# Optimization experiments

Hardware: AMD Instinct MI355X
Metric: run time of the kernel (lower is better)

Reference implementation:

```python
import jax, jax.numpy as jnp
import numpy as np

IDIM = 192
NB_SAMPLES = 128
NB_RAYS = 16384


def setup_inputs() -> dict:
    key = jax.random.key(0)
    k1, k2, k3, k4 = jax.random.split(key, 4)
    # origins strictly inside the AABB [0, idim-1]^3 so every ray intersects
    x = jax.random.uniform(k1, (NB_RAYS, 3), dtype=jnp.float32) * (IDIM - 2.0) + 0.5
    d = jax.random.normal(k2, (NB_RAYS, 3), dtype=jnp.float32)
    # keep components away from 0 so 1/d is finite, then normalize
    d = jnp.where(jnp.abs(d) < 1e-3, 1e-3, d)
    d = d / jnp.linalg.norm(d, axis=1, keepdims=True)
    grid = jax.random.uniform(k3, (IDIM, IDIM, IDIM, 9), dtype=jnp.float32)
    opacity = jax.random.uniform(k4, (IDIM, IDIM, IDIM), dtype=jnp.float32)
    return {"x": x, "d": d, "grid": grid, "opacity": opacity}


def _intersect_ray_aabb(x, inv_d, idim):
    inf = jnp.float32(idim) ** 3
    box_min = jnp.zeros((1, 3), jnp.float32)
    box_max = jnp.full((1, 3), jnp.float32(idim - 1))
    t0 = (box_min - x) * inv_d
    t1 = (box_max - x) * inv_d
    tsmaller = jnp.minimum(t0, t1)
    tbigger = jnp.maximum(t0, t1)
    tmin = jnp.maximum(-inf, jnp.max(tsmaller, axis=1))
    tmax = jnp.minimum(inf, jnp.min(tbigger, axis=1))
    return tmin, tmax


def _forward(x, d, grid, opacity):
    idim = grid.shape[0]
    R = x.shape[0]
    inv_d = 1.0 / d
    tmin, tmax = _intersect_ray_aabb(x, inv_d, idim)
    # Uniform(tmin, tmax) samples, sorted per ray (torch .sample() is no-grad)
    u = jax.random.uniform(jax.random.key(1), (R, NB_SAMPLES), dtype=jnp.float32)
    samples = jnp.sort(tmin[:, None] + u * (tmax - tmin)[:, None], axis=1)
    samples = jax.lax.stop_gradient(samples)

    # sample points along rays: [R, S, 3]
    pts = x[:, None, :] + samples[..., None] * d[:, None, :]
    i0 = jnp.clip(jnp.floor(pts).astype(jnp.int32), 0, idim - 2)  # base corner
    frac = pts - i0.astype(pts.dtype)  # trilinear weights (delta_voxel = 1)
    fx, fy, fz = frac[..., 0], frac[..., 1], frac[..., 2]
    ix, iy, iz = i0[..., 0], i0[..., 1], i0[..., 2]

    harm = jnp.zeros(pts.shape[:2] + (9,), pts.dtype)  # [R, S, 9]
    opac = jnp.zeros(pts.shape[:2], pts.dtype)         # [R, S]
    for ox in (0, 1):
        wx = fx if ox else (1.0 - fx)
        for oy in (0, 1):
            wy = fy if oy else (1.0 - fy)
            for oz in (0, 1):
                wz = fz if oz else (1.0 - fz)
                w = wx * wy * wz
                gi, gj, gk = ix + ox, iy + oy, iz + oz
                harm = harm + w[..., None] * grid[gi, gj, gk]
                opac = opac + w * opacity[gi, gj, gk]

    # volumetric compositing over the first S-1 samples (vectorized form of
    # the original sequential transmittance loop)
    deltas = samples[:, 1:] - samples[:, :-1]            # [R, S-1]
    cur = deltas * opac[:, :-1]                          # per-step opacity
    cum_excl = jnp.concatenate(
        [jnp.zeros((R, 1), cur.dtype), jnp.cumsum(cur, axis=1)[:, :-1]], axis=1)
    trans = jnp.exp(-cum_excl)
    color_s = jax.nn.sigmoid(jnp.sum(harm[:, :-1, :], axis=-1))
    rays_color = jnp.sum(trans * (1.0 - jnp.exp(-cur)) * color_s, axis=1)
    return rays_color


def reference(x, d, grid, opacity):
    return _forward(x, d, grid, opacity)
```

## Files before the change

### kernel.cpp

```cpp
#include <hip/hip_runtime.h>
#include <hip/hip_fp16.h>
#include <cstdint>
#include <cstddef>

#define IDIM 192
#define NSAMP 128
#define NRAYS 16384
#define NVOX (IDIM * IDIM * IDIM)


__device__ __forceinline__ uint32_t rotl32(uint32_t x, int r) {
    return (x << r) | (x >> (32 - r));
}

__device__ __forceinline__ uint32_t threefry_bits(uint32_t i) {
    const uint32_t ks0 = 0u;
    const uint32_t ks1 = 1u;
    const uint32_t ks2 = 0x1BD11BDAu ^ ks0 ^ ks1;
    uint32_t x0 = 0u + ks0;
    uint32_t x1 = i + ks1;
#define TF_ROUND(r) { x0 += x1; x1 = rotl32(x1, (r)); x1 ^= x0; }
    TF_ROUND(13) TF_ROUND(15) TF_ROUND(26) TF_ROUND(6)
    x0 += ks1; x1 += ks2 + 1u;
    TF_ROUND(17) TF_ROUND(29) TF_ROUND(16) TF_ROUND(24)
    x0 += ks2; x1 += ks0 + 2u;
    TF_ROUND(13) TF_ROUND(15) TF_ROUND(26) TF_ROUND(6)
    x0 += ks0; x1 += ks1 + 3u;
    TF_ROUND(17) TF_ROUND(29) TF_ROUND(16) TF_ROUND(24)
    x0 += ks1; x1 += ks2 + 4u;
    TF_ROUND(13) TF_ROUND(15) TF_ROUND(26) TF_ROUND(6)
    x0 += ks2; x1 += ks0 + 5u;
#undef TF_ROUND
    return x0 ^ x1;
}

__global__ __launch_bounds__(256)
void fuse_kernel(const float* __restrict__ grid, const float* __restrict__ opacity,
                 __half2* __restrict__ tab) {
    __shared__ float sh[256 * 9];
    const int t = threadIdx.x;
    const int base = blockIdx.x * 256;
    const float* gp = grid + (size_t)base * 9;
    #pragma unroll
    for (int i = 0; i < 9; ++i) {
        sh[i * 256 + t] = gp[i * 256 + t];
    }
    __syncthreads();
    float s = 0.f;
    #pragma unroll
    for (int c = 0; c < 9; ++c) s += sh[t * 9 + c];
    const int v = base + t;
    const int xq = v / (IDIM * IDIM);
    const int rem = v - xq * (IDIM * IDIM);
    const int yq = rem / IDIM;
    const int zq = rem - yq * IDIM;
    const int idx = (xq >> 1) * 73728 + ((xq & 1) << 3)
                  + (yq >> 1) * 768   + ((yq & 1) << 2)
                  + (zq >> 2) * 16    + (zq & 3);
    tab[idx] = __floats2half2_rn(s, opacity[v]);
}

__global__ __launch_bounds__(128, 8)
void rf_kernel(const float* __restrict__ x, const float* __restrict__ d,
               const __half2* __restrict__ tab, float* __restrict__ out) {
    const int wave = threadIdx.x >> 6;
    const int lane = threadIdx.x & 63;
    const int r = blockIdx.x * 2 + wave;

    const float ox = x[r * 3 + 0], oy = x[r * 3 + 1], oz = x[r * 3 + 2];
    const float dx = d[r * 3 + 0], dy = d[r * 3 + 1], dz = d[r * 3 + 2];
    const float inv_dx = 1.f / dx, inv_dy = 1.f / dy, inv_dz = 1.f / dz;
    const float INF = 7077888.f;
    const float BMAX = (float)(IDIM - 1);

    float tmin = -INF, tmax = INF;
    {
        float t0 = (0.f - ox) * inv_dx, t1 = (BMAX - ox) * inv_dx;
        tmin = fmaxf(tmin, fminf(t0, t1)); tmax = fminf(tmax, fmaxf(t0, t1));
        t0 = (0.f - oy) * inv_dy; t1 = (BMAX - oy) * inv_dy;
        tmin = fmaxf(tmin, fminf(t0, t1)); tmax = fminf(tmax, fmaxf(t0, t1));
        t0 = (0.f - oz) * inv_dz; t1 = (BMAX - oz) * inv_dz;
        tmin = fmaxf(tmin, fminf(t0, t1)); tmax = fminf(tmax, fmaxf(t0, t1));
    }

    const uint32_t i0 = (uint32_t)(r * NSAMP + lane);
    const uint32_t b0 = threefry_bits(i0);
    const uint32_t b1 = threefry_bits(i0 + 64u);
    float u0 = __uint_as_float((b0 >> 9) | 0x3f800000u) - 1.0f;
    float u1 = __uint_as_float((b1 >> 9) | 0x3f800000u) - 1.0f;
    u0 = fmaxf(0.f, u0);
    u1 = fmaxf(0.f, u1);
    float v0 = tmin + u0 * (tmax - tmin);
    float v1 = tmin + u1 * (tmax - tmin);

#define BSTEP(J, K)                                                            \
    {                                                                          \
        const float p0 = __shfl_xor(v0, (J));                                  \
        const float p1 = __shfl_xor(v1, (J));                                  \
        const bool lower = (lane & (J)) == 0;                                  \
        const bool tm0 = (((lane) & (K)) == 0) == lower;                       \
        const bool tm1 = ((((lane) + 64) & (K)) == 0) == lower;                \
        v0 = tm0 ? fminf(v0, p0) : fmaxf(v0, p0);                              \
        v1 = tm1 ? fminf(v1, p1) : fmaxf(v1, p1);                              \
    }
    #pragma unroll
    for (int k = 2; k <= 64; k <<= 1) {
        #pragma unroll
        for (int j = k >> 1; j >= 1; j >>= 1) BSTEP(j, k)
    }
    {
        const float mn = fminf(v0, v1), mx = fmaxf(v0, v1);
        v0 = mn; v1 = mx;
    }
    #pragma unroll
    for (int j = 32; j >= 1; j >>= 1) BSTEP(j, 128)
#undef BSTEP

    auto sample_tab = [&](float tpar, float& hsv, float& opv) {
        const float px = ox + tpar * dx;
        const float py = oy + tpar * dy;
        const float pz = oz + tpar * dz;
        int ix = (int)floorf(px); ix = ix < 0 ? 0 : (ix > IDIM - 2 ? IDIM - 2 : ix);
        int iy = (int)floorf(py); iy = iy < 0 ? 0 : (iy > IDIM - 2 ? IDIM - 2 : iy);
        int iz = (int)floorf(pz); iz = iz < 0 ? 0 : (iz > IDIM - 2 ? IDIM - 2 : iz);
        const float fx = px - (float)ix;
        const float fy = py - (float)iy;
        const float fz = pz - (float)iz;
        const float wx0 = 1.f - fx, wx1 = fx;
        const float wy0 = 1.f - fy, wy1 = fy;
        const float wz0 = 1.f - fz, wz1 = fz;
        const float w000 = wx0 * wy0 * wz0, w001 = wx0 * wy0 * wz1;
        const float w010 = wx0 * wy1 * wz0, w011 = wx0 * wy1 * wz1;
        const float w100 = wx1 * wy0 * wz0, w101 = wx1 * wy0 * wz1;
        const float w110 = wx1 * wy1 * wz0, w111 = wx1 * wy1 * wz1;
        const int f0 = (ix >> 1) * 73728 + ((ix & 1) << 3);
        const int f1 = ((ix + 1) >> 1) * 73728 + (((ix + 1) & 1) << 3);
        const int g0 = (iy >> 1) * 768 + ((iy & 1) << 2);
        const int g1 = ((iy + 1) >> 1) * 768 + (((iy + 1) & 1) << 2);
        const int h0 = (iz >> 2) * 16 + (iz & 3);
        const int h1 = ((iz + 1) >> 2) * 16 + ((iz + 1) & 3);
        const float2 c000 = __half22float2(tab[f0 + g0 + h0]);
        const float2 c001 = __half22float2(tab[f0 + g0 + h1]);
        const float2 c010 = __half22float2(tab[f0 + g1 + h0]);
        const float2 c011 = __half22float2(tab[f0 + g1 + h1]);
        const float2 c100 = __half22float2(tab[f1 + g0 + h0]);
        const float2 c101 = __half22float2(tab[f1 + g0 + h1]);
        const float2 c110 = __half22float2(tab[f1 + g1 + h0]);
        const float2 c111 = __half22float2(tab[f1 + g1 + h1]);
        hsv = w000 * c000.x + w001 * c001.x + w010 * c010.x + w011 * c011.x +
              w100 * c100.x + w101 * c101.x + w110 * c110.x + w111 * c111.x;
        opv = w000 * c000.y + w001 * c001.y + w010 * c010.y + w011 * c011.y +
              w100 * c100.y + w101 * c101.y + w110 * c110.y + w111 * c111.y;
    };

    const float ts = v0;
    const float sd0 = __shfl_down(v0, 1);
    const float b64 = __shfl(v1, 0);
    const float tn = (lane < 63) ? sd0 : b64;

    float hsv, opv;
    sample_tab(ts, hsv, opv);
    const float cur = (tn - ts) * opv;

    float incl = cur;
    #pragma unroll
    for (int off = 1; off < 64; off <<= 1) {
        const float tmp = __shfl_up(incl, off);
        if (lane >= off) incl += tmp;
    }
    const float excl = incl - cur;
    const float color = 1.f / (1.f + __expf(-hsv));
    float contrib = __expf(-excl) * (1.f - __expf(-cur)) * color;

    float red = contrib;
    #pragma unroll
    for (int off = 32; off > 0; off >>= 1) red += __shfl_down(red, off);
    float total = red;

    const float cum64 = __shfl(incl, 63);

    if (cum64 < 10.f) {
        const bool act = lane < 63;
        const float ts2 = v1;
        const float tn2 = __shfl_down(v1, 1);
        float hsv2, opv2;
        sample_tab(ts2, hsv2, opv2);
        const float cur2 = act ? (tn2 - ts2) * opv2 : 0.f;

        float incl2 = cur2;
        #pragma unroll
        for (int off = 1; off < 64; off <<= 1) {
            const float tmp = __shfl_up(incl2, off);
            if (lane >= off) incl2 += tmp;
        }
        const float excl2 = cum64 + (incl2 - cur2);
        const float color2 = 1.f / (1.f + __expf(-hsv2));
        float c2 = act ? __expf(-excl2) * (1.f - __expf(-cur2)) * color2 : 0.f;
        #pragma unroll
        for (int off = 32; off > 0; off >>= 1) c2 += __shfl_down(c2, off);
        total += c2;
    }

    if (lane == 0) out[r] = total;
}

extern "C" void kernel_launch(void* const* d_in, const int* in_sizes, int n_in,
                              void* d_out, int out_size, void* d_ws, size_t ws_size,
                              hipStream_t stream) {
    const float* x       = (const float*)d_in[0];
    const float* d       = (const float*)d_in[1];
    const float* grid    = (const float*)d_in[2];
    const float* opacity = (const float*)d_in[3];
    float* out = (float*)d_out;

    fuse_kernel<<<NVOX / 256, 256, 0, stream>>>(grid, opacity, (__half2*)d_ws);
    rf_kernel<<<NRAYS / 2, 128, 0, stream>>>(x, d, (const __half2*)d_ws, out);
}
```

Baseline: 79.16 us.

## Split trilinear corners across lane pairs and process samples in four chunks

Each pair of lanes now handles one sample: each lane gathers the four corners on its x side and the pair combines partial sums with a lane shuffle. The ray is processed in four chunks of 32 samples with a running transmittance sum and an early exit once accumulated opacity passes a threshold. The intent is to halve the gather work per lane and add finer-grained early termination. In exchange there are more scan passes and shuffles, and half the lanes sit idle in the compositing step.

Measured after the change: 77.90 us. No clear change (-1.6%).

```diff
diff --git a/kernel.cpp b/kernel.cpp
--- a/kernel.cpp
+++ b/kernel.cpp
@@ -116,92 +116,74 @@
     for (int j = 32; j >= 1; j >>= 1) BSTEP(j, 128)
 #undef BSTEP
 
-    auto sample_tab = [&](float tpar, float& hsv, float& opv) {
-        const float px = ox + tpar * dx;
-        const float py = oy + tpar * dy;
-        const float pz = oz + tpar * dz;
+    const int odd = lane & 1;
+    const int hs  = lane >> 1;
+    float cumRay = 0.f, acc = 0.f;
+
+    for (int k = 0; k < 4; ++k) {
+        const int sk = k * 32 + hs;
+        const bool valid = (sk < NSAMP - 1);
+
+        float ts, tn;
+        if (k < 2) {
+            ts = __shfl(v0, sk);
+            const float tnv = __shfl(v0, (sk + 1 > 63) ? 63 : sk + 1);
+            const float s64 = __shfl(v1, 0);
+            tn = (sk == 63) ? s64 : tnv;
+        } else {
+            ts = __shfl(v1, sk - 64);
+            const int ti = sk - 63;
+            tn = __shfl(v1, (ti > 63) ? 63 : ti);
+        }
+
+        const float px = ox + ts * dx;
+        const float py = oy + ts * dy;
+        const float pz = oz + ts * dz;
         int ix = (int)floorf(px); ix = ix < 0 ? 0 : (ix > IDIM - 2 ? IDIM - 2 : ix);
         int iy = (int)floorf(py); iy = iy < 0 ? 0 : (iy > IDIM - 2 ? IDIM - 2 : iy);
         int iz = (int)floorf(pz); iz = iz < 0 ? 0 : (iz > IDIM - 2 ? IDIM - 2 : iz);
         const float fx = px - (float)ix;
         const float fy = py - (float)iy;
         const float fz = pz - (float)iz;
-        const float wx0 = 1.f - fx, wx1 = fx;
+        const float wxs = odd ? fx : (1.f - fx);
         const float wy0 = 1.f - fy, wy1 = fy;
         const float wz0 = 1.f - fz, wz1 = fz;
-        const float w000 = wx0 * wy0 * wz0, w001 = wx0 * wy0 * wz1;
-        const float w010 = wx0 * wy1 * wz0, w011 = wx0 * wy1 * wz1;
-        const float w100 = wx1 * wy0 * wz0, w101 = wx1 * wy0 * wz1;
-        const float w110 = wx1 * wy1 * wz0, w111 = wx1 * wy1 * wz1;
-        const int f0 = (ix >> 1) * 73728 + ((ix & 1) << 3);
-        const int f1 = ((ix + 1) >> 1) * 73728 + (((ix + 1) & 1) << 3);
+        const int xs = ix + odd;
+        const int fs = (xs >> 1) * 73728 + ((xs & 1) << 3);
         const int g0 = (iy >> 1) * 768 + ((iy & 1) << 2);
         const int g1 = ((iy + 1) >> 1) * 768 + (((iy + 1) & 1) << 2);
         const int h0 = (iz >> 2) * 16 + (iz & 3);
         const int h1 = ((iz + 1) >> 2) * 16 + ((iz + 1) & 3);
-        const float2 c000 = __half22float2(tab[f0 + g0 + h0]);
-        const float2 c001 = __half22float2(tab[f0 + g0 + h1]);
-        const float2 c010 = __half22float2(tab[f0 + g1 + h0]);
-        const float2 c011 = __half22float2(tab[f0 + g1 + h1]);
-        const float2 c100 = __half22float2(tab[f1 + g0 + h0]);
-        const float2 c101 = __half22float2(tab[f1 + g0 + h1]);
-        const float2 c110 = __half22float2(tab[f1 + g1 + h0]);
-        const float2 c111 = __half22float2(tab[f1 + g1 + h1]);
-        hsv = w000 * c000.x + w001 * c001.x + w010 * c010.x + w011 * c011.x +
-              w100 * c100.x + w101 * c101.x + w110 * c110.x + w111 * c111.x;
-        opv = w000 * c000.y + w001 * c001.y + w010 * c010.y + w011 * c011.y +
-              w100 * c100.y + w101 * c101.y + w110 * c110.y + w111 * c111.y;
-    };
-
-    const float ts = v0;
-    const float sd0 = __shfl_down(v0, 1);
-    const float b64 = __shfl(v1, 0);
-    const float tn = (lane < 63) ? sd0 : b64;
-
-    float hsv, opv;
-    sample_tab(ts, hsv, opv);
-    const float cur = (tn - ts) * opv;
-
-    float incl = cur;
-    #pragma unroll
-    for (int off = 1; off < 64; off <<= 1) {
-        const float tmp = __shfl_up(incl, off);
-        if (lane >= off) incl += tmp;
-    }
-    const float excl = incl - cur;
-    const float color = 1.f / (1.f + __expf(-hsv));
-    float contrib = __expf(-excl) * (1.f - __expf(-cur)) * color;
-
-    float red = contrib;
-    #pragma unroll
-    for (int off = 32; off > 0; off >>= 1) red += __shfl_down(red, off);
-    float total = red;
-
-    const float cum64 = __shfl(incl, 63);
-
-    if (cum64 < 10.f) {
-        const bool act = lane < 63;
-        const float ts2 = v1;
-        const float tn2 = __shfl_down(v1, 1);
-        float hsv2, opv2;
-        sample_tab(ts2, hsv2, opv2);
-        const float cur2 = act ? (tn2 - ts2) * opv2 : 0.f;
-
-        float incl2 = cur2;
+        const float2 c00 = __half22float2(tab[fs + g0 + h0]);
+        const float2 c01 = __half22float2(tab[fs + g0 + h1]);
+        const float2 c10 = __half22float2(tab[fs + g1 + h0]);
+        const float2 c11 = __half22float2(tab[fs + g1 + h1]);
+        float hp = wxs * (wy0 * (wz0 * c00.x + wz1 * c01.x) +
+                          wy1 * (wz0 * c10.x + wz1 * c11.x));
+        float op = wxs * (wy0 * (wz0 * c00.y + wz1 * c01.y) +
+                          wy1 * (wz0 * c10.y + wz1 * c11.y));
+        const float hsv = hp + __shfl_xor(hp, 1);
+        const float opv = op + __shfl_xor(op, 1);
+
+        const float cur = (valid && !odd) ? (tn - ts) * opv : 0.f;
+        float incl = cur;
         #pragma unroll
         for (int off = 1; off < 64; off <<= 1) {
-            const float tmp = __shfl_up(incl2, off);
-            if (lane >= off) incl2 += tmp;
+            const float tmp = __shfl_up(incl, off);
+            if (lane >= off) incl += tmp;
         }
-        const float excl2 = cum64 + (incl2 - cur2);
-        const float color2 = 1.f / (1.f + __expf(-hsv2));
-        float c2 = act ? __expf(-excl2) * (1.f - __expf(-cur2)) * color2 : 0.f;
-        #pragma unroll
-        for (int off = 32; off > 0; off >>= 1) c2 += __shfl_down(c2, off);
-        total += c2;
-    }
-
-    if (lane == 0) out[r] = total;
+        if (valid && !odd) {
+            const float excl = cumRay + incl - cur;
+            const float color = 1.f / (1.f + __expf(-hsv));
+            acc += __expf(-excl) * (1.f - __expf(-cur)) * color;
+        }
+        cumRay += __shfl(incl, 63);
+        if (cumRay >= 10.f) break;
+    }
+
+    #pragma unroll
+    for (int off = 32; off > 0; off >>= 1) acc += __shfl_down(acc, off);
+    if (lane == 0) out[r] = acc;
 }
 
 extern "C" void kernel_launch(void* const* d_in, const int* in_sizes, int n_in,
```
